# Kernel tuning notes

Hardware: AMD Instinct MI355X
Metric: run time of the kernel (lower is better)

## Reference

```python
import jax, jax.numpy as jnp
import numpy as np

N = 100000
E = 1600000
F_IN = 128
H1, C1 = 8, 8          # conv1: heads=8, hidden_channels=8 -> concat dim 64
H2, C2 = 1, 40         # conv2: heads=1, out=num_classes=40, concat=False
NEG_SLOPE = 0.2
EPS = 1e-16


def setup_inputs() -> dict:
    key = jax.random.key(0)
    ks = jax.random.split(key, 10)
    x = jax.random.normal(ks[0], (N, F_IN), dtype=jnp.float32)
    edge_index = jax.random.randint(ks[1], (2, E), 0, N, dtype=jnp.int32)
    s1 = 1.0 / np.sqrt(F_IN)
    s2 = 1.0 / np.sqrt(H1 * C1)
    W1 = jax.random.normal(ks[2], (F_IN, H1 * C1), dtype=jnp.float32) * s1
    att_src1 = jax.random.normal(ks[3], (H1, C1), dtype=jnp.float32) * s2
    att_dst1 = jax.random.normal(ks[4], (H1, C1), dtype=jnp.float32) * s2
    b1 = jnp.zeros((H1 * C1,), dtype=jnp.float32)
    W2 = jax.random.normal(ks[5], (H1 * C1, H2 * C2), dtype=jnp.float32) * s2
    att_src2 = jax.random.normal(ks[6], (H2, C2), dtype=jnp.float32) * (1.0 / np.sqrt(C2))
    att_dst2 = jax.random.normal(ks[7], (H2, C2), dtype=jnp.float32) * (1.0 / np.sqrt(C2))
    b2 = jnp.zeros((C2,), dtype=jnpp_zeros_dtype()) if False else jnp.zeros((C2,), dtype=jnp.float32)
    return {"x": x, "W1": W1, "att_src1": att_src1, "att_dst1": att_dst1, "b1": b1,
            "W2": W2, "att_src2": att_src2, "att_dst2": att_dst2, "b2": b2,
            "edge_index": edge_index}


def _gat_conv(x, W, att_src, att_dst, bias, src, dst, num_nodes, concat):
    """PyG GATConv (eval mode, self-loops already added to src/dst)."""
    H, C = att_src.shape
    h = (x @ W).reshape(num_nodes, H, C)                 # [N, H, C]
    a_src = jnp.sum(h * att_src[None], axis=-1)          # [N, H]
    a_dst = jnp.sum(h * att_dst[None], axis=-1)          # [N, H]
    e = a_src[src] + a_dst[dst]                          # [Etot, H]
    e = jax.nn.leaky_relu(e, NEG_SLOPE)
    # segment softmax over incoming edges of each dst node
    e_max = jax.ops.segment_max(e, dst, num_segments=num_nodes)   # [N, H]
    ex = jnp.exp(e - e_max[dst])
    denom = jax.ops.segment_sum(ex, dst, num_segments=num_nodes)  # [N, H]
    alpha = ex / (denom[dst] + EPS)                      # [Etot, H]
    msg = h[src] * alpha[..., None]                      # [Etot, H, C]
    out = jax.ops.segment_sum(msg, dst, num_segments=num_nodes)   # [N, H, C]
    if concat:
        out = out.reshape(num_nodes, H * C)
    else:
        out = out.mean(axis=1)
    return out + bias


def reference(x, W1, att_src1, att_dst1, b1, W2, att_src2, att_dst2, b2, edge_index):
    # add self-loops (PyG GATConv default add_self_loops=True)
    loops = jnp.arange(N, dtype=edge_index.dtype)
    src = jnp.concatenate([edge_index[0], loops])
    dst = jnp.concatenate([edge_index[1], loops])
    # dropout layers are identity in eval mode
    emb = jax.nn.elu(_gat_conv(x, W1, att_src1, att_dst1, b1, src, dst, N, True))
    logits = _gat_conv(emb, W2, att_src2, att_dst2, b2, src, dst, N, False)
    return jax.nn.log_softmax(logits, axis=1), emb


def jnp_zeros_dtype():
    return jnp.float32
```

## Files before the change

kernel.cpp:

```cpp
#include <hip/hip_runtime.h>
#include <hip/hip_fp16.h>
#include <math.h>

#define NN 100000
#define EE 1600000
#define ET (EE + NN)
#define FIN 128
#define D1 64
#define H1 8
#define C1 8
#define C2 40
#define NEG 0.2f
#define EPSV 1e-16f
#define LOG2E 1.4426950408889634f

#define NBKT 391
#define BCAP 5120
#define CHUNK 2048
#define NBB ((ET + CHUNK - 1) / CHUNK)
#define G1B ((NN + 63) / 64)
#define PREPB 16

typedef _Float16 f16x8 __attribute__((ext_vector_type(8)));
typedef float f32x4 __attribute__((ext_vector_type(4)));

__device__ __forceinline__ void edge_sd(int e, const int* __restrict__ ei, int& s, int& d) {
  if (e < EE) { s = ei[e]; d = ei[EE + e]; }
  else        { s = e - EE; d = s; }
}

__global__ __launch_bounds__(256) void k1_kernel(
    const int* __restrict__ ei, int* __restrict__ gcur, int* __restrict__ ecsr,
    const float* __restrict__ W1, const float* __restrict__ as1, const float* __restrict__ ad1,
    const float* __restrict__ W2, const float* __restrict__ as2, const float* __restrict__ ad2w,
    __half* __restrict__ Wf1, __half* __restrict__ Wf2) {
  __shared__ int lh[NBKT], lres[NBKT], lcur[NBKT];
  int t = threadIdx.x;
  if (blockIdx.x < NBB) {
    for (int i = t; i < NBKT; i += 256) { lh[i] = 0; lcur[i] = 0; }
    __syncthreads();
    int e0 = blockIdx.x * CHUNK;
    int e1 = min(e0 + CHUNK, ET);
    for (int e = e0 + t; e < e1; e += 256) {
      int d = (e < EE) ? ei[EE + e] : e - EE;
      atomicAdd(&lh[d >> 8], 1);
    }
    __syncthreads();
    for (int i = t; i < NBKT; i += 256)
      if (lh[i]) lres[i] = atomicAdd(&gcur[i], lh[i]);
    __syncthreads();
    for (int e = e0 + t; e < e1; e += 256) {
      int s, d; edge_sd(e, ei, s, d);
      int b = d >> 8;
      int lp = atomicAdd(&lcur[b], 1);
      ecsr[b * BCAP + lres[b] + lp] = s | ((d & 255) << 17);
    }
  } else {
    int gid = (blockIdx.x - NBB) * 256 + t;
    int stride = PREPB * 256;
    for (int idx = gid; idx < 4 * 5 * 64 * 8; idx += stride) {
      int j = idx & 7, l = (idx >> 3) & 63;
      int g = idx >> 9;
      int ct = g % 5, kk = g / 5;
      int kdim = kk * 32 + (l >> 4) * 8 + j;
      int c = l & 15;
      float v;
      if (ct < 4) v = W1[kdim * 64 + ct * 16 + c];
      else {
        const float* aw = (c < 8) ? as1 : ad1;
        int hh = c & 7;
        float acc = 0.f;
        for (int q = 0; q < 8; ++q) acc += W1[kdim * 64 + hh * 8 + q] * aw[hh * 8 + q];
        v = acc * LOG2E;
      }
      Wf1[idx] = __float2half(v);
    }
    for (int idx = gid; idx < 2 * 3 * 64 * 8; idx += stride) {
      int j = idx & 7, l = (idx >> 3) & 63;
      int g = idx >> 9;
      int ct = g % 3, kk = g / 3;
      int kdim = kk * 32 + (l >> 4) * 8 + j;
      int c = ct * 16 + (l & 15);
      float v = 0.f;
      if (c < C2) v = W2[kdim * C2 + c];
      else if (c == 40 || c == 41) {
        const float* aw = (c == 40) ? as2 : ad2w;
        float acc = 0.f;
        for (int q = 0; q < C2; ++q) acc += W2[kdim * C2 + q] * aw[q];
        v = acc * LOG2E;
      }
      Wf2[idx] = __float2half(v);
    }
  }
}

__global__ __launch_bounds__(256) void k2_kernel(
    const int* __restrict__ gcur, int2* __restrict__ rowrng, int* __restrict__ ecsr,
    const float* __restrict__ x, const __half* __restrict__ Wf1,
    __half* __restrict__ h, __half* __restrict__ as_h, float* __restrict__ ad) {
  __shared__ int ebuf[BCAP];
  __shared__ int hist[256];
  __shared__ int sd[256];
  int t = threadIdx.x;
  if (blockIdx.x < NBKT) {
    int b = blockIdx.x;
    int base = b * BCAP;
    int cnt = gcur[b];
    hist[t] = 0;
    __syncthreads();
    for (int i = t; i < cnt; i += 256) {
      int p = ecsr[base + i];
      ebuf[i] = p;
      atomicAdd(&hist[p >> 17], 1);
    }
    __syncthreads();
    int h0 = hist[t];
    sd[t] = h0;
    __syncthreads();
    for (int off = 1; off < 256; off <<= 1) {
      int xv = sd[t];
      int yv = (t >= off) ? sd[t - off] : 0;
      __syncthreads();
      sd[t] = xv + yv;
      __syncthreads();
    }
    int run = sd[t] - h0;
    int g = b * 256 + t;
    if (g < NN) rowrng[g] = make_int2(base + run, base + run + h0);
    hist[t] = run;
    __syncthreads();
    for (int i = t; i < cnt; i += 256) {
      int p = ebuf[i];
      int pos = atomicAdd(&hist[p >> 17], 1);
      ecsr[base + pos] = p & 0x1FFFF;
    }
  } else {
    int blk = blockIdx.x - NBKT;
    int w = t >> 6, lane = t & 63;
    int col = lane & 15, kg = lane >> 4;
    int node0 = blk * 64 + w * 16;
    int nodeA = min(node0 + col, NN - 1);
    const float* xr = x + (size_t)nodeA * FIN + kg * 8;
    const f16x8* Wq = (const f16x8*)Wf1;
    f32x4 acc0 = {0.f,0.f,0.f,0.f}, acc1 = acc0, acc2 = acc0, acc3 = acc0, acc4 = acc0;
#pragma unroll
    for (int kk = 0; kk < 4; ++kk) {
      float4 xa = *(const float4*)(xr + kk * 32);
      float4 xb = *(const float4*)(xr + kk * 32 + 4);
      f16x8 a;
      a[0] = (_Float16)xa.x; a[1] = (_Float16)xa.y; a[2] = (_Float16)xa.z; a[3] = (_Float16)xa.w;
      a[4] = (_Float16)xb.x; a[5] = (_Float16)xb.y; a[6] = (_Float16)xb.z; a[7] = (_Float16)xb.w;
      acc0 = __builtin_amdgcn_mfma_f32_16x16x32_f16(a, Wq[(kk * 5 + 0) * 64 + lane], acc0, 0, 0, 0);
      acc1 = __builtin_amdgcn_mfma_f32_16x16x32_f16(a, Wq[(kk * 5 + 1) * 64 + lane], acc1, 0, 0, 0);
      acc2 = __builtin_amdgcn_mfma_f32_16x16x32_f16(a, Wq[(kk * 5 + 2) * 64 + lane], acc2, 0, 0, 0);
      acc3 = __builtin_amdgcn_mfma_f32_16x16x32_f16(a, Wq[(kk * 5 + 3) * 64 + lane], acc3, 0, 0, 0);
      acc4 = __builtin_amdgcn_mfma_f32_16x16x32_f16(a, Wq[(kk * 5 + 4) * 64 + lane], acc4, 0, 0, 0);
    }
#pragma unroll
    for (int reg = 0; reg < 4; ++reg) {
      int nr = node0 + kg * 4 + reg;
      if (nr < NN) {
        h[(size_t)nr * 64 +  0 + col] = __float2half(acc0[reg]);
        h[(size_t)nr * 64 + 16 + col] = __float2half(acc1[reg]);
        h[(size_t)nr * 64 + 32 + col] = __float2half(acc2[reg]);
        h[(size_t)nr * 64 + 48 + col] = __float2half(acc3[reg]);
        float v = acc4[reg];
        if (col < 8) as_h[nr * 8 + col] = __float2half(v);
        else         ad[nr * 8 + col - 8] = v;
      }
    }
  }
}

#define CONS(u, avh, valid) do { \
    float xx = __half2float(avh) + adv; xx = fmaxf(xx, NEG * xx); \
    float e = (valid) ? exp2f(xx) : 0.f; den += e; \
    float2 f; \
    f = __half22float2(*(const __half2*)&(u).x); a0 = fmaf(f.x, e, a0); a1 = fmaf(f.y, e, a1); \
    f = __half22float2(*(const __half2*)&(u).y); a2 = fmaf(f.x, e, a2); a3 = fmaf(f.y, e, a3); \
    f = __half22float2(*(const __half2*)&(u).z); a4 = fmaf(f.x, e, a4); a5 = fmaf(f.y, e, a5); \
    f = __half22float2(*(const __half2*)&(u).w); a6 = fmaf(f.x, e, a6); a7 = fmaf(f.y, e, a7); \
  } while (0)

__global__ __launch_bounds__(256) void agg1_kernel(
    const int2* __restrict__ rowrng, const int* __restrict__ csr,
    const __half* __restrict__ as_h, const float* __restrict__ ad,
    const __half* __restrict__ h, const float* __restrict__ b1,
    float* __restrict__ emb) {
  int t = threadIdx.x;
  int lane = t & 63;
  int o = lane >> 3, k = lane & 7, ob = lane & 56;
  int node = blockIdx.x * 32 + (t >> 6) * 8 + o;
  int2 rr = rowrng[node];
  int beg = rr.x, deg = rr.y - rr.x, degm1 = deg - 1;
  float adv = ad[node * 8 + k];
  float den = 0.f;
  float a0=0.f,a1=0.f,a2=0.f,a3=0.f,a4=0.f,a5=0.f,a6=0.f,a7=0.f;
  uint4 uA[8]; __half vA[8];
  {
    int sA = csr[beg + min(k, degm1)];
#pragma unroll
    for (int r = 0; r < 8; ++r) {
      int sj = __shfl(sA, ob + r, 64);
      uA[r] = *(const uint4*)(h + ((size_t)(uint)sj << 6) + (k << 3));
      vA[r] = as_h[(uint)sj * 8u + k];
    }
  }
  for (int i = 0; i < deg; i += 16) {
    uint4 uB[8]; __half vB[8];
    bool haveB = (i + 8 < deg);
    if (haveB) {
      int sB = csr[beg + min(i + 8 + k, degm1)];
#pragma unroll
      for (int r = 0; r < 8; ++r) {
        int sj = __shfl(sB, ob + r, 64);
        uB[r] = *(const uint4*)(h + ((size_t)(uint)sj << 6) + (k << 3));
        vB[r] = as_h[(uint)sj * 8u + k];
      }
    }
#pragma unroll
    for (int r = 0; r < 8; ++r) CONS(uA[r], vA[r], i + r < deg);
    if (i + 16 < deg) {
      int sA2 = csr[beg + min(i + 16 + k, degm1)];
#pragma unroll
      for (int r = 0; r < 8; ++r) {
        int sj = __shfl(sA2, ob + r, 64);
        uA[r] = *(const uint4*)(h + ((size_t)(uint)sj << 6) + (k << 3));
        vA[r] = as_h[(uint)sj * 8u + k];
      }
    }
    if (haveB) {
#pragma unroll
      for (int r = 0; r < 8; ++r) CONS(uB[r], vB[r], i + 8 + r < deg);
    }
  }
  float4 bv0 = ((const float4*)b1)[2 * k];
  float4 bv1 = ((const float4*)b1)[2 * k + 1];
  float inv = 1.0f / (den + EPSV);
  float v0 = fmaf(a0, inv, bv0.x), v1 = fmaf(a1, inv, bv0.y);
  float v2 = fmaf(a2, inv, bv0.z), v3 = fmaf(a3, inv, bv0.w);
  float v4 = fmaf(a4, inv, bv1.x), v5 = fmaf(a5, inv, bv1.y);
  float v6 = fmaf(a6, inv, bv1.z), v7 = fmaf(a7, inv, bv1.w);
  v0 = v0 > 0.f ? v0 : expm1f(v0); v1 = v1 > 0.f ? v1 : expm1f(v1);
  v2 = v2 > 0.f ? v2 : expm1f(v2); v3 = v3 > 0.f ? v3 : expm1f(v3);
  v4 = v4 > 0.f ? v4 : expm1f(v4); v5 = v5 > 0.f ? v5 : expm1f(v5);
  v6 = v6 > 0.f ? v6 : expm1f(v6); v7 = v7 > 0.f ? v7 : expm1f(v7);
  float4 s0; s0.x = v0; s0.y = v1; s0.z = v2; s0.w = v3;
  float4 s1; s1.x = v4; s1.y = v5; s1.z = v6; s1.w = v7;
  float* ep = emb + (size_t)node * D1 + (k << 3);
  ((float4*)ep)[0] = s0; ((float4*)ep)[1] = s1;
}

__global__ __launch_bounds__(256) void gemm2_kernel(
    const float* __restrict__ emb, const __half* __restrict__ Wf2,
    __half* __restrict__ h2, float* __restrict__ ad2) {
  int t = threadIdx.x;
  int w = t >> 6, lane = t & 63;
  int col = lane & 15, kg = lane >> 4;
  int node0 = blockIdx.x * 64 + w * 16;
  int nodeA = min(node0 + col, NN - 1);
  const float* er = emb + (size_t)nodeA * D1 + kg * 8;
  const f16x8* Wq = (const f16x8*)Wf2;
  f32x4 acc0 = {0.f,0.f,0.f,0.f}, acc1 = acc0, acc2 = acc0;
#pragma unroll
  for (int kk = 0; kk < 2; ++kk) {
    float4 xa = *(const float4*)(er + kk * 32);
    float4 xb = *(const float4*)(er + kk * 32 + 4);
    f16x8 a;
    a[0] = (_Float16)xa.x; a[1] = (_Float16)xa.y; a[2] = (_Float16)xa.z; a[3] = (_Float16)xa.w;
    a[4] = (_Float16)xb.x; a[5] = (_Float16)xb.y; a[6] = (_Float16)xb.z; a[7] = (_Float16)xb.w;
    acc0 = __builtin_amdgcn_mfma_f32_16x16x32_f16(a, Wq[(kk * 3 + 0) * 64 + lane], acc0, 0, 0, 0);
    acc1 = __builtin_amdgcn_mfma_f32_16x16x32_f16(a, Wq[(kk * 3 + 1) * 64 + lane], acc1, 0, 0, 0);
    acc2 = __builtin_amdgcn_mfma_f32_16x16x32_f16(a, Wq[(kk * 3 + 2) * 64 + lane], acc2, 0, 0, 0);
  }
#pragma unroll
  for (int reg = 0; reg < 4; ++reg) {
    int nr = node0 + kg * 4 + reg;
    if (nr < NN) {
      h2[(size_t)nr * 64 +  0 + col] = __float2half(acc0[reg]);
      h2[(size_t)nr * 64 + 16 + col] = __float2half(acc1[reg]);
      float v = acc2[reg];
      if (col < 8)       h2[(size_t)nr * 64 + 32 + col] = __float2half(v);
      else if (col == 8) h2[(size_t)nr * 64 + 40] = __float2half(v);
      else if (col == 9) ad2[nr] = v;
    }
  }
}

__global__ __launch_bounds__(256) void agg2_kernel(
    const int2* __restrict__ rowrng, const int* __restrict__ csr,
    const float* __restrict__ ad, const __half* __restrict__ h2,
    const float* __restrict__ b2, float* __restrict__ out) {
  int t = threadIdx.x;
  int lane = t & 63;
  int o = lane >> 3, k = lane & 7, ob = lane & 56;
  int kc = min(k, 4);
  int node = blockIdx.x * 32 + (t >> 6) * 8 + o;
  int2 rr = rowrng[node];
  int beg = rr.x, deg = rr.y - rr.x, degm1 = deg - 1;
  float adv = ad[node];
  float den = 0.f;
  float a0=0.f,a1=0.f,a2=0.f,a3=0.f,a4=0.f,a5=0.f,a6=0.f,a7=0.f;
  uint4 uA[8]; __half vA[8];
  {
    int sA = csr[beg + min(k, degm1)];
#pragma unroll
    for (int r = 0; r < 8; ++r) {
      int sj = __shfl(sA, ob + r, 64);
      const __half* rp = h2 + ((size_t)(uint)sj << 6);
      uA[r] = *(const uint4*)(rp + (kc << 3));
      vA[r] = rp[40];
    }
  }
  for (int i = 0; i < deg; i += 16) {
    uint4 uB[8]; __half vB[8];
    bool haveB = (i + 8 < deg);
    if (haveB) {
      int sB = csr[beg + min(i + 8 + k, degm1)];
#pragma unroll
      for (int r = 0; r < 8; ++r) {
        int sj = __shfl(sB, ob + r, 64);
        const __half* rp = h2 + ((size_t)(uint)sj << 6);
        uB[r] = *(const uint4*)(rp + (kc << 3));
        vB[r] = rp[40];
      }
    }
#pragma unroll
    for (int r = 0; r < 8; ++r) CONS(uA[r], vA[r], i + r < deg);
    if (i + 16 < deg) {
      int sA2 = csr[beg + min(i + 16 + k, degm1)];
#pragma unroll
      for (int r = 0; r < 8; ++r) {
        int sj = __shfl(sA2, ob + r, 64);
        const __half* rp = h2 + ((size_t)(uint)sj << 6);
        uA[r] = *(const uint4*)(rp + (kc << 3));
        vA[r] = rp[40];
      }
    }
    if (haveB) {
#pragma unroll
      for (int r = 0; r < 8; ++r) CONS(uB[r], vB[r], i + 8 + r < deg);
    }
  }
  float4 bv0 = ((const float4*)b2)[2 * kc];
  float4 bv1 = ((const float4*)b2)[2 * kc + 1];
  float inv = 1.0f / (den + EPSV);
  float v0 = fmaf(a0, inv, bv0.x), v1 = fmaf(a1, inv, bv0.y);
  float v2 = fmaf(a2, inv, bv0.z), v3 = fmaf(a3, inv, bv0.w);
  float v4 = fmaf(a4, inv, bv1.x), v5 = fmaf(a5, inv, bv1.y);
  float v6 = fmaf(a6, inv, bv1.z), v7 = fmaf(a7, inv, bv1.w);
  bool act = (k < 5);
  float m = act ? fmaxf(fmaxf(fmaxf(v0, v1), fmaxf(v2, v3)),
                        fmaxf(fmaxf(v4, v5), fmaxf(v6, v7))) : -INFINITY;
#pragma unroll
  for (int off = 1; off < 8; off <<= 1) m = fmaxf(m, __shfl_xor(m, off, 64));
  float ex = act ? (__expf(v0 - m) + __expf(v1 - m) + __expf(v2 - m) + __expf(v3 - m) +
                    __expf(v4 - m) + __expf(v5 - m) + __expf(v6 - m) + __expf(v7 - m)) : 0.f;
#pragma unroll
  for (int off = 1; off < 8; off <<= 1) ex += __shfl_xor(ex, off, 64);
  if (act) {
    float lls = m + logf(ex);
    float4 s0; s0.x = v0 - lls; s0.y = v1 - lls; s0.z = v2 - lls; s0.w = v3 - lls;
    float4 s1; s1.x = v4 - lls; s1.y = v5 - lls; s1.z = v6 - lls; s1.w = v7 - lls;
    float* op = out + (size_t)node * C2 + (k << 3);
    ((float4*)op)[0] = s0; ((float4*)op)[1] = s1;
  }
}

extern "C" void kernel_launch(void* const* d_in, const int* in_sizes, int n_in,
                              void* d_out, int out_size, void* d_ws, size_t ws_size,
                              hipStream_t stream) {
  const float* x    = (const float*)d_in[0];
  const float* W1   = (const float*)d_in[1];
  const float* as1w = (const float*)d_in[2];
  const float* ad1w = (const float*)d_in[3];
  const float* b1   = (const float*)d_in[4];
  const float* W2   = (const float*)d_in[5];
  const float* as2w = (const float*)d_in[6];
  const float* ad2w = (const float*)d_in[7];
  const float* b2   = (const float*)d_in[8];
  const int*   ei   = (const int*)d_in[9];

  float* out   = (float*)d_out;
  float* outls = out;
  float* emb   = out + (long)NN * C2;

  char* wsb = (char*)d_ws;
  __half* h1   = (__half*)wsb; wsb += sizeof(__half) * (size_t)NN * D1;
  __half* h2   = (__half*)wsb; wsb += sizeof(__half) * ((size_t)NN * 64 + 64);
  __half* ash1 = (__half*)wsb; wsb += sizeof(__half) * (size_t)NN * H1;
  float* adst1 = (float*)wsb; wsb += sizeof(float) * (size_t)NN * H1;
  float* adst2 = (float*)wsb; wsb += sizeof(float) * (size_t)NN;
  int2* rowrng = (int2*)wsb;  wsb += sizeof(int2) * (size_t)NN;
  int* gcur    = (int*)wsb;   wsb += sizeof(int) * (NBKT + 4);
  __half* Wf1  = (__half*)wsb; wsb += sizeof(__half) * 4 * 5 * 64 * 8;
  __half* Wf2  = (__half*)wsb; wsb += sizeof(__half) * 2 * 3 * 64 * 8;
  int* ecsr    = (int*)wsb;   wsb += sizeof(int) * (size_t)NBKT * BCAP;

  hipMemsetAsync(gcur, 0, sizeof(int) * (NBKT + 4), stream);
  k1_kernel<<<NBB + PREPB, 256, 0, stream>>>(ei, gcur, ecsr,
                                             W1, as1w, ad1w, W2, as2w, ad2w, Wf1, Wf2);
  k2_kernel<<<NBKT + G1B, 256, 0, stream>>>(gcur, rowrng, ecsr, x, Wf1, h1, ash1, adst1);
  agg1_kernel<<<NN / 32, 256, 0, stream>>>(rowrng, ecsr, ash1, adst1, h1, b1, emb);
  gemm2_kernel<<<(NN + 63) / 64, 256, 0, stream>>>(emb, Wf2, h2, adst2);
  agg2_kernel<<<NN / 32, 256, 0, stream>>>(rowrng, ecsr, adst2, h2, b2, outls);
}
```

Before: 257.5 us.

## Sort nodes by degree and pad CSR rows for vectorized index loads

CSR rows are padded to multiples of 8 with a repeated valid source, which lets the aggregation kernels load neighbor indices as aligned int4 vectors instead of shuffling one per lane. A new kernel builds a degree-bucketed permutation of nodes so that each wavefront handles nodes of similar degree, reducing divergence in the per-node loops. This costs an extra kernel launch, atomics for the histogram, a larger CSR buffer, and less locality in output writes because nodes are processed in permuted order.

```diff
diff --git a/kernel.cpp b/kernel.cpp
--- a/kernel.cpp
+++ b/kernel.cpp
@@ -15,11 +15,13 @@
 #define LOG2E 1.4426950408889634f
 
 #define NBKT 391
-#define BCAP 5120
+#define BCAPP 6784
+#define EBUF 5120
 #define CHUNK 2048
 #define NBB ((ET + CHUNK - 1) / CHUNK)
 #define G1B ((NN + 63) / 64)
 #define PREPB 16
+#define DB 32
 
 typedef _Float16 f16x8 __attribute__((ext_vector_type(8)));
 typedef float f32x4 __attribute__((ext_vector_type(4)));
@@ -53,7 +55,7 @@
       int s, d; edge_sd(e, ei, s, d);
       int b = d >> 8;
       int lp = atomicAdd(&lcur[b], 1);
-      ecsr[b * BCAP + lres[b] + lp] = s | ((d & 255) << 17);
+      ecsr[b * BCAPP + lres[b] + lp] = s | ((d & 255) << 17);
     }
   } else {
     int gid = (blockIdx.x - NBB) * 256 + t;
@@ -96,15 +98,16 @@
 
 __global__ __launch_bounds__(256) void k2_kernel(
     const int* __restrict__ gcur, int2* __restrict__ rowrng, int* __restrict__ ecsr,
+    int* __restrict__ dhist,
     const float* __restrict__ x, const __half* __restrict__ Wf1,
     __half* __restrict__ h, __half* __restrict__ as_h, float* __restrict__ ad) {
-  __shared__ int ebuf[BCAP];
+  __shared__ int ebuf[EBUF];
   __shared__ int hist[256];
   __shared__ int sd[256];
   int t = threadIdx.x;
   if (blockIdx.x < NBKT) {
     int b = blockIdx.x;
-    int base = b * BCAP;
+    int base = b * BCAPP;
     int cnt = gcur[b];
     hist[t] = 0;
     __syncthreads();
@@ -115,7 +118,8 @@
     }
     __syncthreads();
     int h0 = hist[t];
-    sd[t] = h0;
+    int p8 = (h0 + 7) & ~7;
+    sd[t] = p8;
     __syncthreads();
     for (int off = 1; off < 256; off <<= 1) {
       int xv = sd[t];
@@ -124,15 +128,23 @@
       sd[t] = xv + yv;
       __syncthreads();
     }
-    int run = sd[t] - h0;
+    int runp = sd[t] - p8;
     int g = b * 256 + t;
-    if (g < NN) rowrng[g] = make_int2(base + run, base + run + h0);
-    hist[t] = run;
+    if (g < NN) {
+      rowrng[g] = make_int2(base + runp, base + runp + h0);
+      atomicAdd(&dhist[min(h0 >> 3, DB - 1)], 1);
+    }
+    hist[t] = runp;
     __syncthreads();
     for (int i = t; i < cnt; i += 256) {
       int p = ebuf[i];
       int pos = atomicAdd(&hist[p >> 17], 1);
       ecsr[base + pos] = p & 0x1FFFF;
+    }
+    __syncthreads();
+    if (g < NN && h0 < p8) {
+      int first = ecsr[base + runp];
+      for (int q = runp + h0; q < runp + p8; ++q) ecsr[base + q] = first;
     }
   } else {
     int blk = blockIdx.x - NBKT;
@@ -172,6 +184,31 @@
   }
 }
 
+__global__ __launch_bounds__(256) void k3_kernel(
+    const int2* __restrict__ rowrng, const int* __restrict__ dhist,
+    int* __restrict__ dcur, int* __restrict__ perm) {
+  __shared__ int lh[DB], lres[DB], lcur[DB];
+  int t = threadIdx.x;
+  if (t < DB) { lh[t] = 0; lcur[t] = 0; }
+  __syncthreads();
+  int n = blockIdx.x * 256 + t;
+  int bkt = 0;
+  if (n < NN) {
+    int2 rr = rowrng[n];
+    bkt = min((rr.y - rr.x) >> 3, DB - 1);
+    atomicAdd(&lh[bkt], 1);
+  }
+  __syncthreads();
+  if (t < DB && lh[t]) lres[t] = atomicAdd(&dcur[t], lh[t]);
+  __syncthreads();
+  if (n < NN) {
+    int lp = atomicAdd(&lcur[bkt], 1);
+    int base = 0;
+    for (int q = 0; q < bkt; ++q) base += dhist[q];
+    perm[base + lres[bkt] + lp] = n;
+  }
+}
+
 #define CONS(u, avh, valid) do { \
     float xx = __half2float(avh) + adv; xx = fmaxf(xx, NEG * xx); \
     float e = (valid) ? exp2f(xx) : 0.f; den += e; \
@@ -182,53 +219,41 @@
     f = __half22float2(*(const __half2*)&(u).w); a6 = fmaf(f.x, e, a6); a7 = fmaf(f.y, e, a7); \
   } while (0)
 
+#define ISSUE1(OFF, U, V) do { \
+    int4 c0_ = *(const int4*)&csr[beg + (OFF)]; \
+    int4 c1_ = *(const int4*)&csr[beg + (OFF) + 4]; \
+    int sj_[8] = {c0_.x, c0_.y, c0_.z, c0_.w, c1_.x, c1_.y, c1_.z, c1_.w}; \
+    _Pragma("unroll") \
+    for (int r_ = 0; r_ < 8; ++r_) { \
+      U[r_] = *(const uint4*)(h + ((size_t)(uint)sj_[r_] << 6) + (k << 3)); \
+      V[r_] = as_h[(uint)sj_[r_] * 8u + k]; \
+    } \
+  } while (0)
+
 __global__ __launch_bounds__(256) void agg1_kernel(
+    const int* __restrict__ perm,
     const int2* __restrict__ rowrng, const int* __restrict__ csr,
     const __half* __restrict__ as_h, const float* __restrict__ ad,
     const __half* __restrict__ h, const float* __restrict__ b1,
     float* __restrict__ emb) {
   int t = threadIdx.x;
   int lane = t & 63;
-  int o = lane >> 3, k = lane & 7, ob = lane & 56;
-  int node = blockIdx.x * 32 + (t >> 6) * 8 + o;
+  int o = lane >> 3, k = lane & 7;
+  int node = perm[blockIdx.x * 32 + (t >> 6) * 8 + o];
   int2 rr = rowrng[node];
-  int beg = rr.x, deg = rr.y - rr.x, degm1 = deg - 1;
+  int beg = rr.x, deg = rr.y - rr.x;
   float adv = ad[node * 8 + k];
   float den = 0.f;
   float a0=0.f,a1=0.f,a2=0.f,a3=0.f,a4=0.f,a5=0.f,a6=0.f,a7=0.f;
   uint4 uA[8]; __half vA[8];
-  {
-    int sA = csr[beg + min(k, degm1)];
-#pragma unroll
-    for (int r = 0; r < 8; ++r) {
-      int sj = __shfl(sA, ob + r, 64);
-      uA[r] = *(const uint4*)(h + ((size_t)(uint)sj << 6) + (k << 3));
-      vA[r] = as_h[(uint)sj * 8u + k];
-    }
-  }
+  ISSUE1(0, uA, vA);
   for (int i = 0; i < deg; i += 16) {
     uint4 uB[8]; __half vB[8];
     bool haveB = (i + 8 < deg);
-    if (haveB) {
-      int sB = csr[beg + min(i + 8 + k, degm1)];
-#pragma unroll
-      for (int r = 0; r < 8; ++r) {
-        int sj = __shfl(sB, ob + r, 64);
-        uB[r] = *(const uint4*)(h + ((size_t)(uint)sj << 6) + (k << 3));
-        vB[r] = as_h[(uint)sj * 8u + k];
-      }
-    }
+    if (haveB) ISSUE1(i + 8, uB, vB);
 #pragma unroll
     for (int r = 0; r < 8; ++r) CONS(uA[r], vA[r], i + r < deg);
-    if (i + 16 < deg) {
-      int sA2 = csr[beg + min(i + 16 + k, degm1)];
-#pragma unroll
-      for (int r = 0; r < 8; ++r) {
-        int sj = __shfl(sA2, ob + r, 64);
-        uA[r] = *(const uint4*)(h + ((size_t)(uint)sj << 6) + (k << 3));
-        vA[r] = as_h[(uint)sj * 8u + k];
-      }
-    }
+    if (i + 16 < deg) ISSUE1(i + 16, uA, vA);
     if (haveB) {
 #pragma unroll
       for (int r = 0; r < 8; ++r) CONS(uB[r], vB[r], i + 8 + r < deg);
@@ -287,56 +312,42 @@
   }
 }
 
+#define ISSUE2(OFF, U, V) do { \
+    int4 c0_ = *(const int4*)&csr[beg + (OFF)]; \
+    int4 c1_ = *(const int4*)&csr[beg + (OFF) + 4]; \
+    int sj_[8] = {c0_.x, c0_.y, c0_.z, c0_.w, c1_.x, c1_.y, c1_.z, c1_.w}; \
+    _Pragma("unroll") \
+    for (int r_ = 0; r_ < 8; ++r_) { \
+      const __half* rp_ = h2 + ((size_t)(uint)sj_[r_] << 6); \
+      U[r_] = *(const uint4*)(rp_ + (kc << 3)); \
+      V[r_] = rp_[40]; \
+    } \
+  } while (0)
+
 __global__ __launch_bounds__(256) void agg2_kernel(
+    const int* __restrict__ perm,
     const int2* __restrict__ rowrng, const int* __restrict__ csr,
     const float* __restrict__ ad, const __half* __restrict__ h2,
     const float* __restrict__ b2, float* __restrict__ out) {
   int t = threadIdx.x;
   int lane = t & 63;
-  int o = lane >> 3, k = lane & 7, ob = lane & 56;
+  int o = lane >> 3, k = lane & 7;
   int kc = min(k, 4);
-  int node = blockIdx.x * 32 + (t >> 6) * 8 + o;
+  int node = perm[blockIdx.x * 32 + (t >> 6) * 8 + o];
   int2 rr = rowrng[node];
-  int beg = rr.x, deg = rr.y - rr.x, degm1 = deg - 1;
+  int beg = rr.x, deg = rr.y - rr.x;
   float adv = ad[node];
   float den = 0.f;
   float a0=0.f,a1=0.f,a2=0.f,a3=0.f,a4=0.f,a5=0.f,a6=0.f,a7=0.f;
   uint4 uA[8]; __half vA[8];
-  {
-    int sA = csr[beg + min(k, degm1)];
-#pragma unroll
-    for (int r = 0; r < 8; ++r) {
-      int sj = __shfl(sA, ob + r, 64);
-      const __half* rp = h2 + ((size_t)(uint)sj << 6);
-      uA[r] = *(const uint4*)(rp + (kc << 3));
-      vA[r] = rp[40];
-    }
-  }
+  ISSUE2(0, uA, vA);
   for (int i = 0; i < deg; i += 16) {
     uint4 uB[8]; __half vB[8];
     bool haveB = (i + 8 < deg);
-    if (haveB) {
-      int sB = csr[beg + min(i + 8 + k, degm1)];
-#pragma unroll
-      for (int r = 0; r < 8; ++r) {
-        int sj = __shfl(sB, ob + r, 64);
-        const __half* rp = h2 + ((size_t)(uint)sj << 6);
-        uB[r] = *(const uint4*)(rp + (kc << 3));
-        vB[r] = rp[40];
-      }
-    }
+    if (haveB) ISSUE2(i + 8, uB, vB);
 #pragma unroll
     for (int r = 0; r < 8; ++r) CONS(uA[r], vA[r], i + r < deg);
-    if (i + 16 < deg) {
-      int sA2 = csr[beg + min(i + 16 + k, degm1)];
-#pragma unroll
-      for (int r = 0; r < 8; ++r) {
-        int sj = __shfl(sA2, ob + r, 64);
-        const __half* rp = h2 + ((size_t)(uint)sj << 6);
-        uA[r] = *(const uint4*)(rp + (kc << 3));
-        vA[r] = rp[40];
-      }
-    }
+    if (i + 16 < deg) ISSUE2(i + 16, uA, vA);
     if (haveB) {
 #pragma unroll
       for (int r = 0; r < 8; ++r) CONS(uB[r], vB[r], i + 8 + r < deg);
@@ -392,16 +403,21 @@
   float* adst1 = (float*)wsb; wsb += sizeof(float) * (size_t)NN * H1;
   float* adst2 = (float*)wsb; wsb += sizeof(float) * (size_t)NN;
   int2* rowrng = (int2*)wsb;  wsb += sizeof(int2) * (size_t)NN;
+  int* perm    = (int*)wsb;   wsb += sizeof(int) * (size_t)NN;
   int* gcur    = (int*)wsb;   wsb += sizeof(int) * (NBKT + 4);
+  int* dhist   = (int*)wsb;   wsb += sizeof(int) * DB;
+  int* dcur    = (int*)wsb;   wsb += sizeof(int) * DB;
   __half* Wf1  = (__half*)wsb; wsb += sizeof(__half) * 4 * 5 * 64 * 8;
   __half* Wf2  = (__half*)wsb; wsb += sizeof(__half) * 2 * 3 * 64 * 8;
-  int* ecsr    = (int*)wsb;   wsb += sizeof(int) * (size_t)NBKT * BCAP;
-
-  hipMemsetAsync(gcur, 0, sizeof(int) * (NBKT + 4), stream);
+  int* ecsr    = (int*)wsb;   wsb += sizeof(int) * (size_t)NBKT * BCAPP;
+
+  hipMemsetAsync(gcur, 0, sizeof(int) * (NBKT + 4 + 2 * DB), stream);
   k1_kernel<<<NBB + PREPB, 256, 0, stream>>>(ei, gcur, ecsr,
                                              W1, as1w, ad1w, W2, as2w, ad2w, Wf1, Wf2);
-  k2_kernel<<<NBKT + G1B, 256, 0, stream>>>(gcur, rowrng, ecsr, x, Wf1, h1, ash1, adst1);
-  agg1_kernel<<<NN / 32, 256, 0, stream>>>(rowrng, ecsr, ash1, adst1, h1, b1, emb);
+  k2_kernel<<<NBKT + G1B, 256, 0, stream>>>(gcur, rowrng, ecsr, dhist,
+                                            x, Wf1, h1, ash1, adst1);
+  k3_kernel<<<(NN + 255) / 256, 256, 0, stream>>>(rowrng, dhist, dcur, perm);
+  agg1_kernel<<<NN / 32, 256, 0, stream>>>(perm, rowrng, ecsr, ash1, adst1, h1, b1, emb);
   gemm2_kernel<<<(NN + 63) / 64, 256, 0, stream>>>(emb, Wf2, h2, adst2);
-  agg2_kernel<<<NN / 32, 256, 0, stream>>>(rowrng, ecsr, adst2, h2, b2, outls);
-}
+  agg2_kernel<<<NN / 32, 256, 0, stream>>>(perm, rowrng, ecsr, adst2, h2, b2, outls);
+}
```

New measurement: 998.7 us. 288% more time.
